# Performance work log

Hardware: AMD Instinct MI355X
Metric: run time of the kernel (lower is better)

## Reference

```python
import jax, jax.numpy as jnp
import numpy as np

BIAS = 0.1  # init kwarg `bias`
B = 8192


def setup_inputs() -> dict:
    key = jax.random.key(0)
    k1, k2, k3 = jax.random.split(key, 3)
    predictions = jax.random.normal(k1, (B,), dtype=jnp.float32)
    correct_output = jax.random.normal(k2, (B,), dtype=jnp.float32)
    weight = jax.random.uniform(k3, (B,), dtype=jnp.float32)
    return {"predictions": predictions, "correct_output": correct_output, "weight": weight}


def reference(predictions, correct_output, weight):
    # pairwise diffs: [B, B], diff[m, n] = pred_m - pred_n
    diff = predictions[:, None] - predictions[None, :]
    gt_diff = correct_output[:, None] - correct_output[None, :]
    # r = +1 if pred_m > pred_n, -1 if pred_m < pred_n, else -sign(gt_m - gt_n)
    r = jnp.where(diff > 0, 1.0, jnp.where(diff < 0, -1.0, -jnp.sign(gt_diff)))
    # weighted by average pair weight
    r = r * (weight[:, None] + weight[None, :]) * 0.5
    loss = jnp.maximum(0.0, BIAS - r * diff)  # hinge per pair
    return jnp.sum(loss) / (B * B)
```

## Files before the change

### kernel.cpp

```cpp
#include <hip/hip_runtime.h>


#define BIAS_F 0.1f

typedef float v2f __attribute__((ext_vector_type(2)));

constexpr int TPB = 256;
constexpr int NPT = 8;
constexpr int NG  = NPT / 2;
constexpr int TN  = TPB * NPT;
constexpr int TM  = 32;

__global__ __launch_bounds__(TPB) void pair_loss_kernel(
    const float* __restrict__ pred,
    const float* __restrict__ weight,
    float* __restrict__ partial,
    int B)
{
    const int n_base = blockIdx.x * TN;
    const int m_base = blockIdx.y * TM;
    const int t = threadIdx.x;

    v2f pn2[NG], wn2[NG], mask2[NG];

    if (n_base + TN <= B) {
        const float4* p4 = reinterpret_cast<const float4*>(pred   + n_base) + 2 * t;
        const float4* w4 = reinterpret_cast<const float4*>(weight + n_base) + 2 * t;
        float4 pa = p4[0], pb = p4[1];
        float4 wa = w4[0], wb = w4[1];
        pn2[0] = (v2f){pa.x, pa.y}; pn2[1] = (v2f){pa.z, pa.w};
        pn2[2] = (v2f){pb.x, pb.y}; pn2[3] = (v2f){pb.z, pb.w};
        wn2[0] = (v2f){wa.x, wa.y} * 0.5f; wn2[1] = (v2f){wa.z, wa.w} * 0.5f;
        wn2[2] = (v2f){wb.x, wb.y} * 0.5f; wn2[3] = (v2f){wb.z, wb.w} * 0.5f;
        #pragma unroll
        for (int j = 0; j < NG; ++j) mask2[j] = (v2f){1.0f, 1.0f};
    } else {
        #pragma unroll
        for (int j = 0; j < NG; ++j) {
            #pragma unroll
            for (int e = 0; e < 2; ++e) {
                int n = n_base + 8 * t + 2 * j + e;
                bool ok = (n < B);
                int nc = ok ? n : 0;
                pn2[j][e]   = pred[nc];
                wn2[j][e]   = weight[nc] * 0.5f;
                mask2[j][e] = ok ? 1.0f : 0.0f;
            }
        }
    }

    v2f acc2[NG];
    #pragma unroll
    for (int j = 0; j < NG; ++j) acc2[j] = (v2f){0.0f, 0.0f};

    const v2f BIAS2 = (v2f){BIAS_F, BIAS_F};
    const int m_end = (m_base + TM <= B) ? TM : (B - m_base);

    #pragma unroll 4
    for (int i = 0; i < m_end; ++i) {
        const int m = m_base + i;
        const float pm  = pred[m];
        const float wmh = weight[m] * 0.5f;
        const v2f pm2 = (v2f){pm, pm};
        const v2f wm2 = (v2f){wmh, wmh};
        #pragma unroll
        for (int j = 0; j < NG; ++j) {
            v2f d  = pm2 - pn2[j];
            v2f w  = wm2 + wn2[j];
            v2f t1 = __builtin_elementwise_fma(-w, d, BIAS2);
            v2f t2 = __builtin_elementwise_fma( w, d, BIAS2);
            v2f h;
            h.x = __builtin_amdgcn_fmed3f(t1.x, t2.x, 0.0f);
            h.y = __builtin_amdgcn_fmed3f(t1.y, t2.y, 0.0f);
            acc2[j] += h;
        }
    }

    float s = 0.0f;
    #pragma unroll
    for (int j = 0; j < NG; ++j)
        s += mask2[j].x * acc2[j].x + mask2[j].y * acc2[j].y;

    #pragma unroll
    for (int off = 32; off > 0; off >>= 1)
        s += __shfl_down(s, off, 64);

    __shared__ float lds[TPB / 64];
    const int lane = t & 63, wid = t >> 6;
    if (lane == 0) lds[wid] = s;
    __syncthreads();
    if (t == 0) {
        float bs = 0.0f;
        #pragma unroll
        for (int w = 0; w < TPB / 64; ++w) bs += lds[w];
        partial[blockIdx.y * gridDim.x + blockIdx.x] = bs;
    }
}

__global__ __launch_bounds__(64) void reduce_kernel(
    const float* __restrict__ partial, int n, float* __restrict__ out, int B)
{
    double s = 0.0;
    for (int i = (int)threadIdx.x; i < n; i += 64) s += (double)partial[i];
    #pragma unroll
    for (int off = 32; off > 0; off >>= 1)
        s += __shfl_down(s, off, 64);
    if (threadIdx.x == 0)
        out[0] = (float)(s / ((double)B * (double)B));
}

extern "C" void kernel_launch(void* const* d_in, const int* in_sizes, int n_in,
                              void* d_out, int out_size, void* d_ws, size_t ws_size,
                              hipStream_t stream) {
    const float* pred   = (const float*)d_in[0];
    const float* weight = (const float*)d_in[2];
    float* out = (float*)d_out;
    const int B = in_sizes[0];

    const int tilesN = (B + TN - 1) / TN;
    const int tilesM = (B + TM - 1) / TM;
    float* partial = (float*)d_ws;

    dim3 grid(tilesN, tilesM);
    pair_loss_kernel<<<grid, TPB, 0, stream>>>(pred, weight, partial, B);
    reduce_kernel<<<1, 64, 0, stream>>>(partial, tilesN * tilesM, out, B);
}
```

Measured before the change: 18.21 us.

## Exploit pair symmetry to compute only the strict upper triangle of pair losses

```diff
diff --git a/kernel.cpp b/kernel.cpp
--- a/kernel.cpp
+++ b/kernel.cpp
@@ -10,41 +10,51 @@
 constexpr int NG  = NPT / 2;
 constexpr int TN  = TPB * NPT;
 constexpr int TM  = 32;
+constexpr int RATIO = TN / TM;
 
-__global__ __launch_bounds__(TPB) void pair_loss_kernel(
+__global__ __launch_bounds__(TPB) void tri_loss_kernel(
     const float* __restrict__ pred,
     const float* __restrict__ weight,
     float* __restrict__ partial,
     int B)
 {
-    const int n_base = blockIdx.x * TN;
-    const int m_base = blockIdx.y * TM;
-    const int t = threadIdx.x;
+    const int tilesM = (B + TM - 1) / TM;
+    const int tilesN = (B + TN - 1) / TN;
 
-    v2f pn2[NG], wn2[NG], mask2[NG];
+    int bid = blockIdx.x;
+    int k = 0, off = 0;
+    for (int kk = 0; kk < tilesN; ++kk) {
+        int len = min(RATIO * (kk + 1), tilesM);
+        if (bid < off + len) { k = kk; break; }
+        off += len;
+    }
+    const int mt = bid - off;
+    const int n0 = k * TN;
+    const int m0 = mt * TM;
+    const int t  = threadIdx.x;
+    const int n_first = n0 + 8 * t;
 
-    if (n_base + TN <= B) {
-        const float4* p4 = reinterpret_cast<const float4*>(pred   + n_base) + 2 * t;
-        const float4* w4 = reinterpret_cast<const float4*>(weight + n_base) + 2 * t;
+    const bool n_in = (n0 + TN <= B);
+
+    v2f pn2[NG], wn2[NG];
+    if (n_in) {
+        const float4* p4 = reinterpret_cast<const float4*>(pred   + n0) + 2 * t;
+        const float4* w4 = reinterpret_cast<const float4*>(weight + n0) + 2 * t;
         float4 pa = p4[0], pb = p4[1];
         float4 wa = w4[0], wb = w4[1];
         pn2[0] = (v2f){pa.x, pa.y}; pn2[1] = (v2f){pa.z, pa.w};
         pn2[2] = (v2f){pb.x, pb.y}; pn2[3] = (v2f){pb.z, pb.w};
         wn2[0] = (v2f){wa.x, wa.y} * 0.5f; wn2[1] = (v2f){wa.z, wa.w} * 0.5f;
         wn2[2] = (v2f){wb.x, wb.y} * 0.5f; wn2[3] = (v2f){wb.z, wb.w} * 0.5f;
-        #pragma unroll
-        for (int j = 0; j < NG; ++j) mask2[j] = (v2f){1.0f, 1.0f};
     } else {
         #pragma unroll
         for (int j = 0; j < NG; ++j) {
             #pragma unroll
             for (int e = 0; e < 2; ++e) {
-                int n = n_base + 8 * t + 2 * j + e;
-                bool ok = (n < B);
-                int nc = ok ? n : 0;
-                pn2[j][e]   = pred[nc];
-                wn2[j][e]   = weight[nc] * 0.5f;
-                mask2[j][e] = ok ? 1.0f : 0.0f;
+                int n = n_first + 2 * j + e;
+                int nc = (n < B) ? n : 0;
+                pn2[j][e] = pred[nc];
+                wn2[j][e] = weight[nc] * 0.5f;
             }
         }
     }
@@ -54,46 +64,86 @@
     for (int j = 0; j < NG; ++j) acc2[j] = (v2f){0.0f, 0.0f};
 
     const v2f BIAS2 = (v2f){BIAS_F, BIAS_F};
-    const int m_end = (m_base + TM <= B) ? TM : (B - m_base);
+    const bool clean = n_in && (m0 + TM <= n0);
 
-    #pragma unroll 4
-    for (int i = 0; i < m_end; ++i) {
-        const int m = m_base + i;
-        const float pm  = pred[m];
-        const float wmh = weight[m] * 0.5f;
-        const v2f pm2 = (v2f){pm, pm};
-        const v2f wm2 = (v2f){wmh, wmh};
-        #pragma unroll
-        for (int j = 0; j < NG; ++j) {
-            v2f d  = pm2 - pn2[j];
-            v2f w  = wm2 + wn2[j];
-            v2f t1 = __builtin_elementwise_fma(-w, d, BIAS2);
-            v2f t2 = __builtin_elementwise_fma( w, d, BIAS2);
-            v2f h;
-            h.x = __builtin_amdgcn_fmed3f(t1.x, t2.x, 0.0f);
-            h.y = __builtin_amdgcn_fmed3f(t1.y, t2.y, 0.0f);
-            acc2[j] += h;
+    if (clean) {
+        #pragma unroll 4
+        for (int i = 0; i < TM; ++i) {
+            const int m = m0 + i;
+            const float pm  = pred[m];
+            const float wmh = weight[m] * 0.5f;
+            const v2f pm2 = (v2f){pm, pm};
+            const v2f wm2 = (v2f){wmh, wmh};
+            #pragma unroll
+            for (int j = 0; j < NG; ++j) {
+                v2f d  = pm2 - pn2[j];
+                v2f w  = wm2 + wn2[j];
+                v2f t1 = __builtin_elementwise_fma(-w, d, BIAS2);
+                v2f t2 = __builtin_elementwise_fma( w, d, BIAS2);
+                v2f h;
+                h.x = __builtin_amdgcn_fmed3f(t1.x, t2.x, 0.0f);
+                h.y = __builtin_amdgcn_fmed3f(t1.y, t2.y, 0.0f);
+                acc2[j] += h;
+            }
+        }
+    } else {
+        const int wid  = __builtin_amdgcn_readfirstlane(t >> 6);
+        const int wnlo = n0 + wid * 512;
+        const int wnhi = wnlo + 511;
+        const int m_end = (m0 + TM <= B) ? TM : (B - m0);
+        for (int i = 0; i < m_end; ++i) {
+            const int m = m0 + i;
+            if (wnhi <= m) continue;
+            const float pm  = pred[m];
+            const float wmh = weight[m] * 0.5f;
+            const v2f pm2 = (v2f){pm, pm};
+            const v2f wm2 = (v2f){wmh, wmh};
+            if (n_in && wnlo > m) {
+                #pragma unroll
+                for (int j = 0; j < NG; ++j) {
+                    v2f d  = pm2 - pn2[j];
+                    v2f w  = wm2 + wn2[j];
+                    v2f t1 = __builtin_elementwise_fma(-w, d, BIAS2);
+                    v2f t2 = __builtin_elementwise_fma( w, d, BIAS2);
+                    v2f h;
+                    h.x = __builtin_amdgcn_fmed3f(t1.x, t2.x, 0.0f);
+                    h.y = __builtin_amdgcn_fmed3f(t1.y, t2.y, 0.0f);
+                    acc2[j] += h;
+                }
+            } else {
+                #pragma unroll
+                for (int j = 0; j < NG; ++j) {
+                    v2f d  = pm2 - pn2[j];
+                    v2f w  = wm2 + wn2[j];
+                    v2f t1 = __builtin_elementwise_fma(-w, d, BIAS2);
+                    v2f t2 = __builtin_elementwise_fma( w, d, BIAS2);
+                    float hx = __builtin_amdgcn_fmed3f(t1.x, t2.x, 0.0f);
+                    float hy = __builtin_amdgcn_fmed3f(t1.y, t2.y, 0.0f);
+                    int nx = n_first + 2 * j, ny = nx + 1;
+                    acc2[j].x += (nx > m && nx < B) ? hx : 0.0f;
+                    acc2[j].y += (ny > m && ny < B) ? hy : 0.0f;
+                }
+            }
         }
     }
 
     float s = 0.0f;
     #pragma unroll
-    for (int j = 0; j < NG; ++j)
-        s += mask2[j].x * acc2[j].x + mask2[j].y * acc2[j].y;
+    for (int j = 0; j < NG; ++j) s += acc2[j].x + acc2[j].y;
 
     #pragma unroll
-    for (int off = 32; off > 0; off >>= 1)
-        s += __shfl_down(s, off, 64);
+    for (int off2 = 32; off2 > 0; off2 >>= 1)
+        s += __shfl_down(s, off2, 64);
 
     __shared__ float lds[TPB / 64];
-    const int lane = t & 63, wid = t >> 6;
-    if (lane == 0) lds[wid] = s;
+    const int lane = t & 63, wid2 = t >> 6;
+    if (lane == 0) lds[wid2] = s;
     __syncthreads();
     if (t == 0) {
         float bs = 0.0f;
         #pragma unroll
         for (int w = 0; w < TPB / 64; ++w) bs += lds[w];
-        partial[blockIdx.y * gridDim.x + blockIdx.x] = bs;
+        partial[bid] = bs;
     }
 }
 
@@ -105,8 +155,10 @@
     #pragma unroll
     for (int off = 32; off > 0; off >>= 1)
         s += __shfl_down(s, off, 64);
-    if (threadIdx.x == 0)
-        out[0] = (float)(s / ((double)B * (double)B));
+    if (threadIdx.x == 0) {
+        double full = 2.0 * s + (double)B * (double)BIAS_F;
+        out[0] = (float)(full / ((double)B * (double)B));
+    }
 }
 
 extern "C" void kernel_launch(void* const* d_in, const int* in_sizes, int n_in,
@@ -117,11 +169,16 @@
     float* out = (float*)d_out;
     const int B = in_sizes[0];
 
+    const int tilesM = (B + TM - 1) / TM;
     const int tilesN = (B + TN - 1) / TN;
-    const int tilesM = (B + TM - 1) / TM;
+    int nActive = 0;
+    for (int k = 0; k < tilesN; ++k) {
+        int len = RATIO * (k + 1);
+        if (len > tilesM) len = tilesM;
+        nActive += len;
+    }
     float* partial = (float*)d_ws;
 
-    dim3 grid(tilesN, tilesM);
-    pair_loss_kernel<<<grid, TPB, 0, stream>>>(pred, weight, partial, B);
-    reduce_kernel<<<1, 64, 0, stream>>>(partial, tilesN * tilesM, out, B);
+    tri_loss_kernel<<<nActive, TPB, 0, stream>>>(pred, weight, partial, B);
+    reduce_kernel<<<1, 64, 0, stream>>>(partial, nActive, out, B);
 }
```

Result: slower. 21.33 us (+17.2%).
